# Optimization experiments

Measured on AMD Instinct MI355X. Metric: run time of the kernel, lower is better.

Reference implementation:

```python
import jax, jax.numpy as jnp
import numpy as np

N_NODES = 50000
N_EDGES = 800000
IN_DIM = 128
HID_DIM = 256
OUT_DIM = 128


def _sage_conv(x, edge_index, W_l, b_l, W_r):
    """PyG SAGEConv with mean aggregation:
       out_i = W_l @ mean_{j in N(i)} x_j + b_l + W_r @ x_i
    edge_index: [2, E] with row 0 = source j, row 1 = target i."""
    src, dst = edge_index[0], edge_index[1]
    n = x.shape[0]
    # gather source features along edges, scatter-sum into targets
    msg_sum = jax.ops.segment_sum(x[src], dst, num_segments=n)  # [N, D]
    deg = jax.ops.segment_sum(jnp.ones((src.shape[0],), dtype=x.dtype), dst,
                              num_segments=n)                    # [N]
    msg_mean = msg_sum / jnp.maximum(deg, 1.0)[:, None]
    return msg_mean @ W_l.T + b_l + x @ W_r.T


def setup_inputs() -> dict:
    key = jax.random.key(0)
    ks = jax.random.split(key, 8)
    x = jax.random.normal(ks[0], (N_NODES, IN_DIM), dtype=jnp.float32)
    edge_index = jax.random.randint(ks[1], (2, N_EDGES), 0, N_NODES, dtype=jnp.int64)
    # glorot-ish scaled params
    def w(k, shape):
        fan_in = shape[-1]
        return jax.random.normal(k, shape, dtype=jnp.float32) / np.sqrt(fan_in)
    W1_l = w(ks[2], (HID_DIM, IN_DIM))
    W1_r = w(ks[3], (HID_DIM, IN_DIM))
    b1 = jnp.zeros((HID_DIM,), dtype=jnp.float32)
    W2_l = w(ks[4], (OUT_DIM, HID_DIM))
    W2_r = w(ks[5], (OUT_DIM, HID_DIM))
    b2 = jnp.zeros((OUT_DIM,), dtype=jnp.float32)
    return {"x": x, "edge_index": edge_index,
            "W1_l": W1_l, "b1": b1, "W1_r": W1_r,
            "W2_l": W2_l, "b2": b2, "W2_r": W2_r}


def reference(x, edge_index, W1_l, b1, W1_r, W2_l, b2, W2_r):
    h = _sage_conv(x, edge_index, W1_l, b1, W1_r)
    h = jax.nn.relu(h)
    # dropout(p=0.3) is identity in inference mode
    out = _sage_conv(h, edge_index, W2_l, b2, W2_r)
    return out
```

## Files before the change

### kernel.cpp

```cpp
#include <hip/hip_runtime.h>
#include <stdint.h>

#define NN 50000
#define NE 800000
#define NBK 512
#define NPB 98
#define BUCKCAP 2048

typedef __bf16 bf16x8 __attribute__((ext_vector_type(8)));
typedef float  f32x4  __attribute__((ext_vector_type(4)));

__device__ __forceinline__ unsigned short f2bf(float f) {
    unsigned int u = __float_as_uint(f);
    unsigned int r = (u + 0x7fffu + ((u >> 16) & 1u)) >> 16;
    return (unsigned short)r;
}
__device__ __forceinline__ float bf_lo(unsigned int v) { return __uint_as_float(v << 16); }
__device__ __forceinline__ float bf_hi(unsigned int v) { return __uint_as_float(v & 0xffff0000u); }

__device__ __forceinline__ void gl_lds16(const void* g, void* l) {
    __builtin_amdgcn_global_load_lds(
        (const __attribute__((address_space(1))) void*)g,
        (__attribute__((address_space(3))) void*)l, 16, 0, 0);
}

#define FILL_NB 391
#define PACK_NB 512
#define CAST_NB 6250
__global__ __launch_bounds__(256) void mega_kernel(
    const int* __restrict__ edges,
    int* __restrict__ bcur, unsigned int* __restrict__ packed,
    const float* __restrict__ x, unsigned short* __restrict__ x_bf,
    const float* __restrict__ W1l, const float* __restrict__ W1r,
    const float* __restrict__ W2l, const float* __restrict__ W2r,
    unsigned short* __restrict__ B1, unsigned short* __restrict__ B2) {
    __shared__ int hist[NBK];
    __shared__ int scn[NBK];
    __shared__ int gbase[NBK];
    __shared__ int lcur[NBK];
    __shared__ int ps[256];
    __shared__ unsigned int sortbuf[2048];
    __shared__ int gaddrbuf[2048];
    __shared__ int nz;
    int b = blockIdx.x;
    int t = threadIdx.x;
    if (b < FILL_NB) {
        const int E = NE;
        if (t == 0) nz = 0;
        hist[t] = 0; hist[t + 256] = 0;
        __syncthreads();
        int accv = 0;
        for (int i = t; i < 512; i += 256) accv |= edges[2 * i + 1];
        if (accv) atomicOr(&nz, 1);
        __syncthreads();
        int f = nz ? 0 : 1;

        int blockbase = b * 2048;
        int nedge = E - blockbase; if (nedge > 2048) nedge = 2048;
        unsigned int pk[8]; int bk[8];
#pragma unroll
        for (int u = 0; u < 8; ++u) {
            int lin = u * 256 + t;
            bk[u] = -1;
            if (lin < nedge) {
                int e = blockbase + lin;
                int src = edges[(size_t)e << f];
                int dst = edges[(size_t)(E + e) << f];
                int bb = dst / NPB;
                pk[u] = (unsigned int)src | ((unsigned int)(dst - bb * NPB) << 16);
                bk[u] = bb;
                atomicAdd(&hist[bb], 1);
            }
        }
        __syncthreads();
        int h0 = hist[2 * t], h1 = hist[2 * t + 1];
        int s = h0 + h1;
        ps[t] = s;
        __syncthreads();
        for (int off = 1; off < 256; off <<= 1) {
            int v = (t >= off) ? ps[t - off] : 0;
            __syncthreads();
            ps[t] += v;
            __syncthreads();
        }
        int excl = ps[t] - s;
        scn[2 * t] = excl;
        scn[2 * t + 1] = excl + h0;
        if (h0) gbase[2 * t] = atomicAdd(&bcur[2 * t], h0);
        if (h1) gbase[2 * t + 1] = atomicAdd(&bcur[2 * t + 1], h1);
        lcur[2 * t] = excl;
        lcur[2 * t + 1] = excl + h0;
        __syncthreads();
#pragma unroll
        for (int u = 0; u < 8; ++u) {
            if (bk[u] >= 0) {
                int p = atomicAdd(&lcur[bk[u]], 1);
                sortbuf[p] = pk[u];
                int off = gbase[bk[u]] + (p - scn[bk[u]]);
                gaddrbuf[p] = (off < BUCKCAP) ? (bk[u] * BUCKCAP + off) : -1;
            }
        }
        __syncthreads();
        for (int j = t; j < nedge; j += 256) {
            int a = gaddrbuf[j];
            if (a >= 0) packed[a] = sortbuf[j];
        }
    } else if (b < FILL_NB + PACK_NB) {
        int idx = (b - FILL_NB) * 256 + t;
        if (idx < 65536) {
            int o = idx >> 8, k = idx & 255;
            float v = (k < 128) ? W1l[o * 128 + k] : W1r[o * 128 + (k - 128)];
            B1[idx] = f2bf(v);
        } else {
            int j = idx - 65536;
            int o = j >> 8, k = j & 255;
            float v = (o < 128) ? W2l[o * 256 + k] : W2r[(o - 128) * 256 + k];
            B2[j] = f2bf(v);
        }
    } else {
        int i4 = (b - FILL_NB - PACK_NB) * 256 + t;
        float4 v = *(const float4*)(x + (size_t)i4 * 4);
        uint2 p;
        p.x = (unsigned int)f2bf(v.x) | ((unsigned int)f2bf(v.y) << 16);
        p.y = (unsigned int)f2bf(v.z) | ((unsigned int)f2bf(v.w) << 16);
        *(uint2*)(x_bf + (size_t)i4 * 4) = p;
    }
}

__global__ __launch_bounds__(512) void pass2agg1_kernel(
    const unsigned int* __restrict__ packed, const int* __restrict__ bcur,
    const unsigned short* __restrict__ X,
    unsigned short* __restrict__ nbr, int* __restrict__ row_start, int* __restrict__ deg,
    unsigned short* __restrict__ mean) {
    __shared__ int hist[NPB];
    __shared__ int scn[NPB];
    __shared__ int lcur[NPB];
    __shared__ unsigned short lists[BUCKCAP];
    __shared__ int nodectr;
    int b = blockIdx.x;
    int t = threadIdx.x;
    int ne = bcur[b]; if (ne > BUCKCAP) ne = BUCKCAP;
    if (t < NPB) hist[t] = 0;
    if (t == 0) nodectr = 0;
    __syncthreads();
    const unsigned int* pb = packed + (size_t)b * BUCKCAP;
    for (int j = t; j < ne; j += 512) atomicAdd(&hist[pb[j] >> 16], 1);
    __syncthreads();
    if (t == 0) {
        int a = 0;
        for (int i = 0; i < NPB; ++i) { scn[i] = a; a += hist[i]; }
    }
    __syncthreads();
    if (t < NPB) lcur[t] = scn[t];
    __syncthreads();
    for (int j = t; j < ne; j += 512) {
        unsigned int w = pb[j];
        int p = atomicAdd(&lcur[w >> 16], 1);
        lists[p] = (unsigned short)(w & 0xffffu);
    }
    __syncthreads();
    if (t < NPB) {
        int node = b * NPB + t;
        if (node < NN) {
            row_start[node] = b * BUCKCAP + scn[t];
            deg[node] = hist[t];
        }
    }
    for (int j = t; j < ne; j += 512) nbr[(size_t)b * BUCKCAP + j] = lists[j];
    int l = t & 15;
    for (;;) {
        int n = 0;
        if (l == 0) n = atomicAdd(&nodectr, 1);
        n = __shfl(n, 0, 16);
        if (n >= NPB) break;
        int node = b * NPB + n;
        if (node >= NN) break;
        int dg = hist[n];
        const unsigned short* sl = &lists[scn[n]];
        float a0 = 0.f, a1 = 0.f, a2 = 0.f, a3 = 0.f, a4 = 0.f, a5 = 0.f, a6 = 0.f, a7 = 0.f;
        int i = 0;
        for (; i + 8 <= dg; i += 8) {
            uint4 v[8];
#pragma unroll
            for (int u = 0; u < 8; ++u) {
                int s = sl[i + u];
                v[u] = *(const uint4*)(X + ((size_t)s << 7) + l * 8);
            }
#pragma unroll
            for (int u = 0; u < 8; ++u) {
                a0 += bf_lo(v[u].x); a1 += bf_hi(v[u].x);
                a2 += bf_lo(v[u].y); a3 += bf_hi(v[u].y);
                a4 += bf_lo(v[u].z); a5 += bf_hi(v[u].z);
                a6 += bf_lo(v[u].w); a7 += bf_hi(v[u].w);
            }
        }
        for (; i < dg; ++i) {
            int s = sl[i];
            uint4 v = *(const uint4*)(X + ((size_t)s << 7) + l * 8);
            a0 += bf_lo(v.x); a1 += bf_hi(v.x);
            a2 += bf_lo(v.y); a3 += bf_hi(v.y);
            a4 += bf_lo(v.z); a5 += bf_hi(v.z);
            a6 += bf_lo(v.w); a7 += bf_hi(v.w);
        }
        float inv = 1.0f / (float)(dg > 1 ? dg : 1);
        uint4 p;
        p.x = (unsigned int)f2bf(a0 * inv) | ((unsigned int)f2bf(a1 * inv) << 16);
        p.y = (unsigned int)f2bf(a2 * inv) | ((unsigned int)f2bf(a3 * inv) << 16);
        p.z = (unsigned int)f2bf(a4 * inv) | ((unsigned int)f2bf(a5 * inv) << 16);
        p.w = (unsigned int)f2bf(a6 * inv) | ((unsigned int)f2bf(a7 * inv) << 16);
        *(uint4*)(mean + ((size_t)node << 7) + l * 8) = p;
    }
}

__global__ __launch_bounds__(512) void gemm_mfma(
    const unsigned short* __restrict__ A1, const unsigned short* __restrict__ A2,
    int astr1, int astr2,
    const unsigned short* __restrict__ B,
    const float* __restrict__ biasBF, const float* __restrict__ biasF,
    unsigned short* __restrict__ outBF, float* __restrict__ outF,
    int N, int split, int reluBF) {
    __shared__ unsigned short As[128 * 64];
    __shared__ unsigned short Bs[256 * 64];
    int tid = threadIdx.x;
    int row0 = blockIdx.x * 128;
    int w = tid >> 6, lane = tid & 63;
    int wr = w >> 2, wc = w & 3;
    int q = lane >> 4, l16 = lane & 15;
    int rc = lane >> 3;
    int gsw = (lane & 7) ^ (rc & 7);

    f32x4 acc[4][4];
#pragma unroll
    for (int r = 0; r < 4; ++r)
#pragma unroll
        for (int c = 0; c < 4; ++c) acc[r][c] = (f32x4){0.f, 0.f, 0.f, 0.f};

    for (int ks = 0; ks < 4; ++ks) {
        int kbase = ks * 64;
        if (ks) __syncthreads();
        const unsigned short* Ap = (ks < 2) ? A1 : A2;
        int astr = (ks < 2) ? astr1 : astr2;
        int koff = (ks & 1) * 64;
#pragma unroll
        for (int cc = 0; cc < 2; ++cc) {
            int c = w * 2 + cc;
            int grow = row0 + c * 8 + rc;
            if (grow > N - 1) grow = N - 1;
            gl_lds16(Ap + (size_t)grow * astr + koff + gsw * 8, &As[c * 512]);
        }
#pragma unroll
        for (int cc = 0; cc < 4; ++cc) {
            int c = w * 4 + cc;
            int n = c * 8 + rc;
            gl_lds16(B + ((size_t)n << 8) + kbase + gsw * 8, &Bs[c * 512]);
        }
        __syncthreads();
#pragma unroll
        for (int k0 = 0; k0 < 64; k0 += 32) {
            int gb = (k0 >> 3) + q;
            int sl = gb ^ (l16 & 7);
            bf16x8 bfrag[4], afrag[4];
#pragma unroll
            for (int c = 0; c < 4; ++c) {
                int row = wc * 64 + c * 16 + l16;
                bfrag[c] = *(const bf16x8*)&Bs[row * 64 + sl * 8];
            }
#pragma unroll
            for (int r = 0; r < 4; ++r) {
                int row = wr * 64 + r * 16 + l16;
                afrag[r] = *(const bf16x8*)&As[row * 64 + sl * 8];
            }
#pragma unroll
            for (int r = 0; r < 4; ++r)
#pragma unroll
                for (int c = 0; c < 4; ++c)
                    acc[r][c] = __builtin_amdgcn_mfma_f32_16x16x32_bf16(afrag[r], bfrag[c], acc[r][c], 0, 0, 0);
        }
    }

#pragma unroll
    for (int c = 0; c < 4; ++c) {
        int colg = wc * 64 + c * 16 + l16;
        bool isBF = (colg < split);
        float bb = 0.f;
        if (isBF) { if (biasBF) bb = biasBF[colg]; }
        else      bb = biasF[colg - split];
#pragma unroll
        for (int r = 0; r < 4; ++r) {
#pragma unroll
            for (int reg = 0; reg < 4; ++reg) {
                int rowg = row0 + wr * 64 + r * 16 + q * 4 + reg;
                if (rowg < N) {
                    float v = acc[r][c][reg] + bb;
                    if (isBF) {
                        if (reluBF) v = fmaxf(v, 0.f);
                        outBF[(size_t)rowg * split + colg] = f2bf(v);
                    } else {
                        outF[(size_t)rowg * (256 - split) + (colg - split)] = v;
                    }
                }
            }
        }
    }
}

__global__ __launch_bounds__(256) void agg2_kernel(
    const unsigned short* __restrict__ P, const float* __restrict__ R,
    const int* __restrict__ row_start, const int* __restrict__ deg,
    const unsigned short* __restrict__ nbr, float* __restrict__ out) {
    __shared__ unsigned short ll[16][80];
    int w = threadIdx.x >> 4;
    int l = threadIdx.x & 15;
    int node = blockIdx.x * 16 + w;
    if (node >= NN) return;
    int dg = deg[node];
    const unsigned short* gsl = nbr + row_start[node];
    float a0 = 0.f, a1 = 0.f, a2 = 0.f, a3 = 0.f, a4 = 0.f, a5 = 0.f, a6 = 0.f, a7 = 0.f;
    if (dg <= 80) {
        for (int i = l; i < dg; i += 16) ll[w][i] = gsl[i];
        __builtin_amdgcn_wave_barrier();
        const unsigned short* sl = &ll[w][0];
        int i = 0;
        for (; i + 8 <= dg; i += 8) {
            uint4 v[8];
#pragma unroll
            for (int u = 0; u < 8; ++u) {
                int s = sl[i + u];
                v[u] = *(const uint4*)(P + ((size_t)s << 7) + l * 8);
            }
#pragma unroll
            for (int u = 0; u < 8; ++u) {
                a0 += bf_lo(v[u].x); a1 += bf_hi(v[u].x);
                a2 += bf_lo(v[u].y); a3 += bf_hi(v[u].y);
                a4 += bf_lo(v[u].z); a5 += bf_hi(v[u].z);
                a6 += bf_lo(v[u].w); a7 += bf_hi(v[u].w);
            }
        }
        for (; i < dg; ++i) {
            int s = sl[i];
            uint4 v = *(const uint4*)(P + ((size_t)s << 7) + l * 8);
            a0 += bf_lo(v.x); a1 += bf_hi(v.x);
            a2 += bf_lo(v.y); a3 += bf_hi(v.y);
            a4 += bf_lo(v.z); a5 += bf_hi(v.z);
            a6 += bf_lo(v.w); a7 += bf_hi(v.w);
        }
    } else {
        for (int i = 0; i < dg; ++i) {
            int s = gsl[i];
            uint4 v = *(const uint4*)(P + ((size_t)s << 7) + l * 8);
            a0 += bf_lo(v.x); a1 += bf_hi(v.x);
            a2 += bf_lo(v.y); a3 += bf_hi(v.y);
            a4 += bf_lo(v.z); a5 += bf_hi(v.z);
            a6 += bf_lo(v.w); a7 += bf_hi(v.w);
        }
    }
    float inv = 1.0f / (float)(dg > 1 ? dg : 1);
    const float* rrow = R + ((size_t)node << 7) + l * 8;
    float4 r0 = *(const float4*)rrow;
    float4 r1 = *(const float4*)(rrow + 4);
    float4 o0, o1;
    o0.x = a0 * inv + r0.x; o0.y = a1 * inv + r0.y;
    o0.z = a2 * inv + r0.z; o0.w = a3 * inv + r0.w;
    o1.x = a4 * inv + r1.x; o1.y = a5 * inv + r1.y;
    o1.z = a6 * inv + r1.z; o1.w = a7 * inv + r1.w;
    float* orow = out + ((size_t)node << 7) + l * 8;
    *(float4*)orow = o0;
    *(float4*)(orow + 4) = o1;
}

extern "C" void kernel_launch(void* const* d_in, const int* in_sizes, int n_in,
                              void* d_out, int out_size, void* d_ws, size_t ws_size,
                              hipStream_t stream) {
    const float* x    = (const float*)d_in[0];
    const int*   edges = (const int*)d_in[1];
    const float* W1_l = (const float*)d_in[2];
    const float* b1   = (const float*)d_in[3];
    const float* W1_r = (const float*)d_in[4];
    const float* W2_l = (const float*)d_in[5];
    const float* b2   = (const float*)d_in[6];
    const float* W2_r = (const float*)d_in[7];
    float* out = (float*)d_out;

    const int N = NN;
    auto al = [](size_t v) { return (v + 255) & ~(size_t)255; };
    char* ws = (char*)d_ws;
    size_t o = 0;
    int* bcur = (int*)(ws + o); o += al((size_t)NBK * 4);
    unsigned int* packed = (unsigned int*)(ws + o); o += al((size_t)NBK * BUCKCAP * 4);
    unsigned short* nbr = (unsigned short*)(ws + o); o += al((size_t)NBK * BUCKCAP * 2);
    int* row_start = (int*)(ws + o); o += al((size_t)N * 4);
    int* deg       = (int*)(ws + o); o += al((size_t)N * 4);
    unsigned short* x_bf  = (unsigned short*)(ws + o); o += al((size_t)N * 128 * 2);
    unsigned short* mean1 = (unsigned short*)(ws + o); o += al((size_t)N * 128 * 2);
    unsigned short* h_bf  = (unsigned short*)(ws + o); o += al((size_t)N * 256 * 2);
    unsigned short* P_bf  = (unsigned short*)(ws + o); o += al((size_t)N * 128 * 2);
    float*          R_f   = (float*)(ws + o);          o += al((size_t)N * 128 * 4);
    unsigned short* B1    = (unsigned short*)(ws + o); o += al((size_t)256 * 256 * 2);
    unsigned short* B2    = (unsigned short*)(ws + o); o += al((size_t)256 * 256 * 2);

    hipMemsetAsync(bcur, 0, (size_t)NBK * sizeof(int), stream);
    mega_kernel<<<FILL_NB + PACK_NB + CAST_NB, 256, 0, stream>>>(
        edges, bcur, packed, x, x_bf, W1_l, W1_r, W2_l, W2_r, B1, B2);
    pass2agg1_kernel<<<NBK, 512, 0, stream>>>(packed, bcur, x_bf, nbr, row_start, deg, mean1);
    gemm_mfma<<<(N + 127) / 128, 512, 0, stream>>>(mean1, x_bf, 128, 128, B1, b1, b1,
                                                   h_bf, (float*)nullptr, N, 256, 1);
    gemm_mfma<<<(N + 127) / 128, 512, 0, stream>>>(h_bf, h_bf + 128, 256, 256, B2,
                                                   (float*)nullptr, b2, P_bf, R_f, N, 128, 0);
    agg2_kernel<<<(N + 15) / 16, 256, 0, stream>>>(P_bf, R_f, row_start, deg, nbr, out);
}
```

Before: 212.2 us.

## Split aggregation by feature slices mapped to XCDs for L2 locality

Separates the neighbor-mean aggregation from the CSR build kernel and rewrites both aggregation kernels so each block handles a 32-column feature slice over a node chunk. Blocks are indexed so that each pair of XCDs (by blockIdx mod 8) works on a single feature slice, meaning each XCD's L2 only needs to cache a quarter of the gathered feature matrix. The aim is more L2 hits on the random gathers. In exchange it adds a kernel launch, re-reads the neighbor lists and degrees four times, and moves smaller 16-byte segments per node.

New measurement: 237.4 us. 11.8% more time.

```diff
diff --git a/kernel.cpp b/kernel.cpp
--- a/kernel.cpp
+++ b/kernel.cpp
@@ -127,21 +127,17 @@
     }
 }
 
-__global__ __launch_bounds__(512) void pass2agg1_kernel(
+__global__ __launch_bounds__(512) void pass2_kernel(
     const unsigned int* __restrict__ packed, const int* __restrict__ bcur,
-    const unsigned short* __restrict__ X,
-    unsigned short* __restrict__ nbr, int* __restrict__ row_start, int* __restrict__ deg,
-    unsigned short* __restrict__ mean) {
+    unsigned short* __restrict__ nbr, int* __restrict__ row_start, int* __restrict__ deg) {
     __shared__ int hist[NPB];
     __shared__ int scn[NPB];
     __shared__ int lcur[NPB];
     __shared__ unsigned short lists[BUCKCAP];
-    __shared__ int nodectr;
     int b = blockIdx.x;
     int t = threadIdx.x;
     int ne = bcur[b]; if (ne > BUCKCAP) ne = BUCKCAP;
     if (t < NPB) hist[t] = 0;
-    if (t == 0) nodectr = 0;
     __syncthreads();
     const unsigned int* pb = packed + (size_t)b * BUCKCAP;
     for (int j = t; j < ne; j += 512) atomicAdd(&hist[pb[j] >> 16], 1);
@@ -167,24 +163,46 @@
         }
     }
     for (int j = t; j < ne; j += 512) nbr[(size_t)b * BUCKCAP + j] = lists[j];
-    int l = t & 15;
-    for (;;) {
-        int n = 0;
-        if (l == 0) n = atomicAdd(&nodectr, 1);
-        n = __shfl(n, 0, 16);
-        if (n >= NPB) break;
-        int node = b * NPB + n;
-        if (node >= NN) break;
-        int dg = hist[n];
-        const unsigned short* sl = &lists[scn[n]];
+}
+
+#define AGG_G 128
+#define AGG_CH ((NN + 2*AGG_G - 1) / (2*AGG_G))
+
+__global__ __launch_bounds__(256) void agg1s_kernel(
+    const unsigned short* __restrict__ X,
+    const int* __restrict__ row_start, const int* __restrict__ deg,
+    const unsigned short* __restrict__ nbr,
+    unsigned short* __restrict__ mean) {
+    __shared__ unsigned short ll[64][80];
+    int b = blockIdx.x;
+    int xcd = b & 7;
+    int slice = xcd >> 1;
+    int chunk = (xcd & 1) * AGG_G + (b >> 3);
+    int t = threadIdx.x;
+    int wk = t >> 2;
+    int l = t & 3;
+    int n0 = chunk * AGG_CH;
+    int n1 = n0 + AGG_CH; if (n1 > NN) n1 = NN;
+    int co = slice * 32 + l * 8;
+    for (int node = n0 + wk; node < n1; node += 64) {
+        int dg = deg[node];
+        const unsigned short* gsl = nbr + row_start[node];
         float a0 = 0.f, a1 = 0.f, a2 = 0.f, a3 = 0.f, a4 = 0.f, a5 = 0.f, a6 = 0.f, a7 = 0.f;
+        const unsigned short* sl;
+        if (dg <= 80) {
+            for (int i = l; i < dg; i += 4) ll[wk][i] = gsl[i];
+            __builtin_amdgcn_wave_barrier();
+            sl = &ll[wk][0];
+        } else {
+            sl = gsl;
+        }
         int i = 0;
         for (; i + 8 <= dg; i += 8) {
             uint4 v[8];
 #pragma unroll
             for (int u = 0; u < 8; ++u) {
                 int s = sl[i + u];
-                v[u] = *(const uint4*)(X + ((size_t)s << 7) + l * 8);
+                v[u] = *(const uint4*)(X + ((size_t)s << 7) + co);
             }
 #pragma unroll
             for (int u = 0; u < 8; ++u) {
@@ -196,7 +214,7 @@
         }
         for (; i < dg; ++i) {
             int s = sl[i];
-            uint4 v = *(const uint4*)(X + ((size_t)s << 7) + l * 8);
+            uint4 v = *(const uint4*)(X + ((size_t)s << 7) + co);
             a0 += bf_lo(v.x); a1 += bf_hi(v.x);
             a2 += bf_lo(v.y); a3 += bf_hi(v.y);
             a4 += bf_lo(v.z); a5 += bf_hi(v.z);
@@ -208,7 +226,73 @@
         p.y = (unsigned int)f2bf(a2 * inv) | ((unsigned int)f2bf(a3 * inv) << 16);
         p.z = (unsigned int)f2bf(a4 * inv) | ((unsigned int)f2bf(a5 * inv) << 16);
         p.w = (unsigned int)f2bf(a6 * inv) | ((unsigned int)f2bf(a7 * inv) << 16);
-        *(uint4*)(mean + ((size_t)node << 7) + l * 8) = p;
+        *(uint4*)(mean + ((size_t)node << 7) + co) = p;
+    }
+}
+
+__global__ __launch_bounds__(256) void agg2s_kernel(
+    const unsigned short* __restrict__ P, const float* __restrict__ R,
+    const int* __restrict__ row_start, const int* __restrict__ deg,
+    const unsigned short* __restrict__ nbr, float* __restrict__ out) {
+    __shared__ unsigned short ll[64][80];
+    int b = blockIdx.x;
+    int xcd = b & 7;
+    int slice = xcd >> 1;
+    int chunk = (xcd & 1) * AGG_G + (b >> 3);
+    int t = threadIdx.x;
+    int wk = t >> 2;
+    int l = t & 3;
+    int n0 = chunk * AGG_CH;
+    int n1 = n0 + AGG_CH; if (n1 > NN) n1 = NN;
+    int co = slice * 32 + l * 8;
+    for (int node = n0 + wk; node < n1; node += 64) {
+        int dg = deg[node];
+        const unsigned short* gsl = nbr + row_start[node];
+        float a0 = 0.f, a1 = 0.f, a2 = 0.f, a3 = 0.f, a4 = 0.f, a5 = 0.f, a6 = 0.f, a7 = 0.f;
+        const unsigned short* sl;
+        if (dg <= 80) {
+            for (int i = l; i < dg; i += 4) ll[wk][i] = gsl[i];
+            __builtin_amdgcn_wave_barrier();
+            sl = &ll[wk][0];
+        } else {
+            sl = gsl;
+        }
+        int i = 0;
+        for (; i + 8 <= dg; i += 8) {
+            uint4 v[8];
+#pragma unroll
+            for (int u = 0; u < 8; ++u) {
+                int s = sl[i + u];
+                v[u] = *(const uint4*)(P + ((size_t)s << 7) + co);
+            }
+#pragma unroll
+            for (int u = 0; u < 8; ++u) {
+                a0 += bf_lo(v[u].x); a1 += bf_hi(v[u].x);
+                a2 += bf_lo(v[u].y); a3 += bf_hi(v[u].y);
+                a4 += bf_lo(v[u].z); a5 += bf_hi(v[u].z);
+                a6 += bf_lo(v[u].w); a7 += bf_hi(v[u].w);
+            }
+        }
+        for (; i < dg; ++i) {
+            int s = sl[i];
+            uint4 v = *(const uint4*)(P + ((size_t)s << 7) + co);
+            a0 += bf_lo(v.x); a1 += bf_hi(v.x);
+            a2 += bf_lo(v.y); a3 += bf_hi(v.y);
+            a4 += bf_lo(v.z); a5 += bf_hi(v.z);
+            a6 += bf_lo(v.w); a7 += bf_hi(v.w);
+        }
+        float inv = 1.0f / (float)(dg > 1 ? dg : 1);
+        const float* rrow = R + ((size_t)node << 7) + co;
+        float4 r0 = *(const float4*)rrow;
+        float4 r1 = *(const float4*)(rrow + 4);
+        float4 o0, o1;
+        o0.x = a0 * inv + r0.x; o0.y = a1 * inv + r0.y;
+        o0.z = a2 * inv + r0.z; o0.w = a3 * inv + r0.w;
+        o1.x = a4 * inv + r1.x; o1.y = a5 * inv + r1.y;
+        o1.z = a6 * inv + r1.z; o1.w = a7 * inv + r1.w;
+        float* orow = out + ((size_t)node << 7) + co;
+        *(float4*)orow = o0;
+        *(float4*)(orow + 4) = o1;
     }
 }
 
@@ -304,70 +388,6 @@
     }
 }
 
-__global__ __launch_bounds__(256) void agg2_kernel(
-    const unsigned short* __restrict__ P, const float* __restrict__ R,
-    const int* __restrict__ row_start, const int* __restrict__ deg,
-    const unsigned short* __restrict__ nbr, float* __restrict__ out) {
-    __shared__ unsigned short ll[16][80];
-    int w = threadIdx.x >> 4;
-    int l = threadIdx.x & 15;
-    int node = blockIdx.x * 16 + w;
-    if (node >= NN) return;
-    int dg = deg[node];
-    const unsigned short* gsl = nbr + row_start[node];
-    float a0 = 0.f, a1 = 0.f, a2 = 0.f, a3 = 0.f, a4 = 0.f, a5 = 0.f, a6 = 0.f, a7 = 0.f;
-    if (dg <= 80) {
-        for (int i = l; i < dg; i += 16) ll[w][i] = gsl[i];
-        __builtin_amdgcn_wave_barrier();
-        const unsigned short* sl = &ll[w][0];
-        int i = 0;
-        for (; i + 8 <= dg; i += 8) {
-            uint4 v[8];
-#pragma unroll
-            for (int u = 0; u < 8; ++u) {
-                int s = sl[i + u];
-                v[u] = *(const uint4*)(P + ((size_t)s << 7) + l * 8);
-            }
-#pragma unroll
-            for (int u = 0; u < 8; ++u) {
-                a0 += bf_lo(v[u].x); a1 += bf_hi(v[u].x);
-                a2 += bf_lo(v[u].y); a3 += bf_hi(v[u].y);
-                a4 += bf_lo(v[u].z); a5 += bf_hi(v[u].z);
-                a6 += bf_lo(v[u].w); a7 += bf_hi(v[u].w);
-            }
-        }
-        for (; i < dg; ++i) {
-            int s = sl[i];
-            uint4 v = *(const uint4*)(P + ((size_t)s << 7) + l * 8);
-            a0 += bf_lo(v.x); a1 += bf_hi(v.x);
-            a2 += bf_lo(v.y); a3 += bf_hi(v.y);
-            a4 += bf_lo(v.z); a5 += bf_hi(v.z);
-            a6 += bf_lo(v.w); a7 += bf_hi(v.w);
-        }
-    } else {
-        for (int i = 0; i < dg; ++i) {
-            int s = gsl[i];
-            uint4 v = *(const uint4*)(P + ((size_t)s << 7) + l * 8);
-            a0 += bf_lo(v.x); a1 += bf_hi(v.x);
-            a2 += bf_lo(v.y); a3 += bf_hi(v.y);
-            a4 += bf_lo(v.z); a5 += bf_hi(v.z);
-            a6 += bf_lo(v.w); a7 += bf_hi(v.w);
-        }
-    }
-    float inv = 1.0f / (float)(dg > 1 ? dg : 1);
-    const float* rrow = R + ((size_t)node << 7) + l * 8;
-    float4 r0 = *(const float4*)rrow;
-    float4 r1 = *(const float4*)(rrow + 4);
-    float4 o0, o1;
-    o0.x = a0 * inv + r0.x; o0.y = a1 * inv + r0.y;
-    o0.z = a2 * inv + r0.z; o0.w = a3 * inv + r0.w;
-    o1.x = a4 * inv + r1.x; o1.y = a5 * inv + r1.y;
-    o1.z = a6 * inv + r1.z; o1.w = a7 * inv + r1.w;
-    float* orow = out + ((size_t)node << 7) + l * 8;
-    *(float4*)orow = o0;
-    *(float4*)(orow + 4) = o1;
-}
-
 extern "C" void kernel_launch(void* const* d_in, const int* in_sizes, int n_in,
                               void* d_out, int out_size, void* d_ws, size_t ws_size,
                               hipStream_t stream) {
@@ -401,10 +421,11 @@
     hipMemsetAsync(bcur, 0, (size_t)NBK * sizeof(int), stream);
     mega_kernel<<<FILL_NB + PACK_NB + CAST_NB, 256, 0, stream>>>(
         edges, bcur, packed, x, x_bf, W1_l, W1_r, W2_l, W2_r, B1, B2);
-    pass2agg1_kernel<<<NBK, 512, 0, stream>>>(packed, bcur, x_bf, nbr, row_start, deg, mean1);
+    pass2_kernel<<<NBK, 512, 0, stream>>>(packed, bcur, nbr, row_start, deg);
+    agg1s_kernel<<<8 * AGG_G, 256, 0, stream>>>(x_bf, row_start, deg, nbr, mean1);
     gemm_mfma<<<(N + 127) / 128, 512, 0, stream>>>(mean1, x_bf, 128, 128, B1, b1, b1,
                                                    h_bf, (float*)nullptr, N, 256, 1);
     gemm_mfma<<<(N + 127) / 128, 512, 0, stream>>>(h_bf, h_bf + 128, 256, 256, B2,
                                                    (float*)nullptr, b2, P_bf, R_f, N, 128, 0);
-    agg2_kernel<<<(N + 15) / 16, 256, 0, stream>>>(P_bf, R_f, row_start, deg, nbr, out);
-}
+    agg2s_kernel<<<8 * AGG_G, 256, 0, stream>>>(P_bf, R_f, row_start, deg, nbr, out);
+}
```
